# Optimization experiments

Hardware: AMD Instinct MI355X
Metric: run time of the kernel (lower is better)

## Reference

```python
import jax, jax.numpy as jnp
import numpy as np

ALPHA = 0.5  # args.alpha in the original script
N_NODES = 100000   # line-graph nodes == edges of the original graph
N_EDGES = 1600000  # line-graph edges (non-backtracking adjacency)
D = 128

def setup_inputs() -> dict:
    key = jax.random.key(0)
    k1, k2, k3 = jax.random.split(key, 3)
    edge_feats = jax.random.normal(k1, (N_NODES, D), dtype=jnp.float32)
    src = jax.random.randint(k2, (N_EDGES,), 0, N_NODES, dtype=jnp.int32)
    dst = jax.random.randint(k3, (N_EDGES,), 0, N_NODES, dtype=jnp.int32)
    return {"edge_feats": edge_feats, "src": src, "dst": dst}

def reference(edge_feats, src, dst):
    # copy_u: gather source-node features along line-graph edges
    msg = edge_feats[src]                                   # [E, D]
    n = edge_feats.shape[0]
    # mean reduce per destination node; zero-degree nodes -> 0 (DGL semantics)
    s = jax.ops.segment_sum(msg, dst, num_segments=n)       # [N, D]
    cnt = jax.ops.segment_sum(jnp.ones((src.shape[0],), edge_feats.dtype), dst, num_segments=n)
    h_new = s / jnp.maximum(cnt, 1.0)[:, None]
    # alpha-weighted residual mix
    return ALPHA * edge_feats + (1.0 - ALPHA) * h_new
```

## Files before the change

### kernel.cpp

```cpp
#include <hip/hip_runtime.h>
#include <hip/hip_fp16.h>

#define NN 100000
#define NE 1600000
#define NBKT 782
#define CHUNK 8192
#define NBLK1 196
#define DIRW (NBKT + 1)
#define CAPB 2432
#define CVTBLK 604
#define GRID1 (NBLK1 + CVTBLK)

#define OFF_DIR   0
#define OFF_PAIRS 153600
#define OFF_F16   (OFF_PAIRS + NBLK1 * CHUNK)
#define WORDS_ALL (OFF_F16 + NN * 64)

__global__ __launch_bounds__(512) void bin_convert_kernel(
        const int* __restrict__ src, const int* __restrict__ dst,
        const float2* __restrict__ feats2,
        unsigned* __restrict__ pairs1, int* __restrict__ dir,
        __half2* __restrict__ f16, int fp16on) {
    __shared__ unsigned stage[CHUNK];
    __shared__ int hist[NBKT];
    __shared__ int bbase[NBKT];
    __shared__ int curs[NBKT];
    __shared__ int tsum[512];
    const int tid = threadIdx.x;
    const int blk = blockIdx.x;

    if (blk >= NBLK1) {
        if (fp16on) {
            const int cb = blk - NBLK1;
            for (int i = cb * 512 + tid; i < NN * 64; i += CVTBLK * 512)
                f16[i] = __float22half2_rn(feats2[i]);
        }
        return;
    }

    const int e0 = blk * CHUNK;
    const int n = min(CHUNK, NE - e0);

    for (int b = tid; b < NBKT; b += 512) hist[b] = 0;
    __syncthreads();
    for (int i = tid; i < n; i += 512)
        atomicAdd(&hist[dst[e0 + i] >> 7], 1);
    __syncthreads();

    const int b0 = tid * 2, b1 = tid * 2 + 1;
    const int v0 = (b0 < NBKT) ? hist[b0] : 0;
    const int v1 = (b1 < NBKT) ? hist[b1] : 0;
    tsum[tid] = v0 + v1;
    __syncthreads();
    for (int st = 1; st < 512; st <<= 1) {
        int t = (tid >= st) ? tsum[tid - st] : 0;
        __syncthreads();
        tsum[tid] += t;
        __syncthreads();
    }
    const int tb = tsum[tid] - (v0 + v1);
    if (b0 < NBKT) { bbase[b0] = tb;      curs[b0] = tb; }
    if (b1 < NBKT) { bbase[b1] = tb + v0; curs[b1] = tb + v0; }
    __syncthreads();

    for (int i = tid; i < n; i += 512) {
        const int d = dst[e0 + i];
        const int sv = src[e0 + i];
        const int pos = atomicAdd(&curs[d >> 7], 1);
        stage[pos] = ((unsigned)sv << 7) | (unsigned)(d & 127);
    }
    __syncthreads();

    unsigned* gp = pairs1 + (size_t)blk * CHUNK;
    for (int i = tid; i < n; i += 512) gp[i] = stage[i];
    int* dp = dir + (size_t)blk * DIRW;
    for (int b = tid; b < NBKT; b += 512) dp[b] = bbase[b];
    if (tid == 0) dp[NBKT] = n;
}

__global__ __launch_bounds__(256) void gather_kernel(
        const float2* __restrict__ feats2,
        const __half2* __restrict__ f16,
        const unsigned* __restrict__ pairs1,
        const int* __restrict__ dir,
        float2* __restrict__ out2, int fp16on) {
    __shared__ unsigned pairs_s[CAPB];
    __shared__ int idx_s[CAPB];
    __shared__ int rbase[NBLK1], rlen[NBLK1], rdst[NBLK1];
    __shared__ int scan_t[256];
    __shared__ int hist[128], offs[128], curs[128];
    __shared__ int total_s;

    const int b = blockIdx.x;
    const int tid = threadIdx.x;
    const int node0 = b << 7;
    const int nNodes = min(128, NN - node0);

    int cj = 0;
    if (tid < NBLK1) {
        const int* dp = dir + (size_t)tid * DIRW + b;
        const int s0 = dp[0];
        const int s1 = dp[1];
        rbase[tid] = s0;
        cj = s1 - s0;
        rlen[tid] = cj;
    }
    scan_t[tid] = cj;
    __syncthreads();
    for (int st = 1; st < 256; st <<= 1) {
        int t = (tid >= st) ? scan_t[tid - st] : 0;
        __syncthreads();
        scan_t[tid] += t;
        __syncthreads();
    }
    if (tid < NBLK1) rdst[tid] = scan_t[tid] - cj;
    if (tid == 255) total_s = scan_t[255];
    __syncthreads();
    const int cnt = min(total_s, CAPB);

    const int sub = tid >> 5, lane32 = tid & 31;
    for (int j = sub; j < NBLK1; j += 8) {
        const int len = rlen[j];
        const int gb = rbase[j];
        const int db = rdst[j];
        const unsigned* gp = pairs1 + (size_t)j * CHUNK + gb;
        for (int k = lane32; k < len; k += 32) {
            const int dpos = db + k;
            if (dpos < CAPB) pairs_s[dpos] = gp[k];
        }
    }
    if (tid < 128) hist[tid] = 0;
    __syncthreads();

    for (int i = tid; i < cnt; i += 256) atomicAdd(&hist[pairs_s[i] & 127], 1);
    __syncthreads();

    if (tid < 128) curs[tid] = hist[tid];
    __syncthreads();
    for (int st = 1; st < 128; st <<= 1) {
        int t = (tid < 128 && tid >= st) ? curs[tid - st] : 0;
        __syncthreads();
        if (tid < 128) curs[tid] += t;
        __syncthreads();
    }
    if (tid < 128) {
        const int ex = curs[tid] - hist[tid];
        offs[tid] = ex;
        curs[tid] = ex;
    }
    __syncthreads();
    for (int i = tid; i < cnt; i += 256) {
        const unsigned p = pairs_s[i];
        const int pos = atomicAdd(&curs[p & 127], 1);
        idx_s[pos] = (int)(p >> 7);
    }
    __syncthreads();

    const int lane = tid & 63;
    const int w = tid >> 6;
    for (int dl = w; dl < nNodes; dl += 4) {
        const int start = offs[dl];
        const int deg = hist[dl];
        float2 acc = make_float2(0.f, 0.f);
        int j = 0;
        if (fp16on) {
            for (; j + 3 < deg; j += 4) {
                const int s0 = idx_s[start + j + 0];
                const int s1 = idx_s[start + j + 1];
                const int s2 = idx_s[start + j + 2];
                const int s3 = idx_s[start + j + 3];
                const float2 v0 = __half22float2(f16[(size_t)s0 * 64 + lane]);
                const float2 v1 = __half22float2(f16[(size_t)s1 * 64 + lane]);
                const float2 v2 = __half22float2(f16[(size_t)s2 * 64 + lane]);
                const float2 v3 = __half22float2(f16[(size_t)s3 * 64 + lane]);
                acc.x += v0.x + v1.x + v2.x + v3.x;
                acc.y += v0.y + v1.y + v2.y + v3.y;
            }
            for (; j < deg; ++j) {
                const float2 v = __half22float2(f16[(size_t)idx_s[start + j] * 64 + lane]);
                acc.x += v.x; acc.y += v.y;
            }
        } else {
            for (; j + 3 < deg; j += 4) {
                const int s0 = idx_s[start + j + 0];
                const int s1 = idx_s[start + j + 1];
                const int s2 = idx_s[start + j + 2];
                const int s3 = idx_s[start + j + 3];
                const float2 v0 = feats2[(size_t)s0 * 64 + lane];
                const float2 v1 = feats2[(size_t)s1 * 64 + lane];
                const float2 v2 = feats2[(size_t)s2 * 64 + lane];
                const float2 v3 = feats2[(size_t)s3 * 64 + lane];
                acc.x += v0.x + v1.x + v2.x + v3.x;
                acc.y += v0.y + v1.y + v2.y + v3.y;
            }
            for (; j < deg; ++j) {
                const float2 v = feats2[(size_t)idx_s[start + j] * 64 + lane];
                acc.x += v.x; acc.y += v.y;
            }
        }
        const int node = node0 + dl;
        const float inv = 0.5f / fmaxf((float)deg, 1.0f);
        const float2 f = feats2[(size_t)node * 64 + lane];
        out2[(size_t)node * 64 + lane] =
            make_float2(0.5f * f.x + inv * acc.x, 0.5f * f.y + inv * acc.y);
    }
}

extern "C" void kernel_launch(void* const* d_in, const int* in_sizes, int n_in,
                              void* d_out, int out_size, void* d_ws, size_t ws_size,
                              hipStream_t stream) {
    const float* feats = (const float*)d_in[0];
    const int*   src   = (const int*)d_in[1];
    const int*   dst   = (const int*)d_in[2];
    float* out = (float*)d_out;

    int*      ws_i   = (int*)d_ws;
    int*      dir    = ws_i + OFF_DIR;
    unsigned* pairs1 = (unsigned*)(ws_i + OFF_PAIRS);
    __half2*  f16    = (__half2*)(ws_i + OFF_F16);
    const int fp16on = (ws_size >= (size_t)WORDS_ALL * 4u) ? 1 : 0;

    bin_convert_kernel<<<GRID1, 512, 0, stream>>>(
        src, dst, (const float2*)feats, pairs1, dir, f16, fp16on);
    gather_kernel<<<NBKT, 256, 0, stream>>>(
        (const float2*)feats, f16, pairs1, dir, (float2*)out, fp16on);
}
```

Measured before the change: 207.9 us.

## Halve bin chunks, use wave-shuffle scans, unroll gather, read residual from fp16

The binning kernel now uses 4096-edge chunks with 391 blocks of 256 threads and fewer conversion blocks. Both kernels replace the barrier-heavy shared-memory prefix scans with wavefront shuffle scans plus a small cross-wave total. The gather unrolls the fp16 path to 8 loads in flight and reads the residual term from the fp16 copy instead of fp32. The trade-off is that the gather must now merge 391 directory runs per bucket, and the residual term loses precision by coming from fp16.

```diff
diff --git a/kernel.cpp b/kernel.cpp
--- a/kernel.cpp
+++ b/kernel.cpp
@@ -4,19 +4,19 @@
 #define NN 100000
 #define NE 1600000
 #define NBKT 782
-#define CHUNK 8192
-#define NBLK1 196
+#define CHUNK 4096
+#define NBLK1 391
 #define DIRW (NBKT + 1)
 #define CAPB 2432
-#define CVTBLK 604
+#define CVTBLK 409
 #define GRID1 (NBLK1 + CVTBLK)
 
 #define OFF_DIR   0
-#define OFF_PAIRS 153600
+#define OFF_PAIRS 306176
 #define OFF_F16   (OFF_PAIRS + NBLK1 * CHUNK)
 #define WORDS_ALL (OFF_F16 + NN * 64)
 
-__global__ __launch_bounds__(512) void bin_convert_kernel(
+__global__ __launch_bounds__(256) void bin_convert_kernel(
         const int* __restrict__ src, const int* __restrict__ dst,
         const float2* __restrict__ feats2,
         unsigned* __restrict__ pairs1, int* __restrict__ dir,
@@ -25,14 +25,14 @@
     __shared__ int hist[NBKT];
     __shared__ int bbase[NBKT];
     __shared__ int curs[NBKT];
-    __shared__ int tsum[512];
+    __shared__ int wtot[4];
     const int tid = threadIdx.x;
     const int blk = blockIdx.x;
 
     if (blk >= NBLK1) {
         if (fp16on) {
             const int cb = blk - NBLK1;
-            for (int i = cb * 512 + tid; i < NN * 64; i += CVTBLK * 512)
+            for (int i = cb * 256 + tid; i < NN * 64; i += CVTBLK * 256)
                 f16[i] = __float22half2_rn(feats2[i]);
         }
         return;
@@ -41,29 +41,39 @@
     const int e0 = blk * CHUNK;
     const int n = min(CHUNK, NE - e0);
 
-    for (int b = tid; b < NBKT; b += 512) hist[b] = 0;
-    __syncthreads();
-    for (int i = tid; i < n; i += 512)
+    for (int b = tid; b < NBKT; b += 256) hist[b] = 0;
+    __syncthreads();
+    for (int i = tid; i < n; i += 256)
         atomicAdd(&hist[dst[e0 + i] >> 7], 1);
     __syncthreads();
 
-    const int b0 = tid * 2, b1 = tid * 2 + 1;
-    const int v0 = (b0 < NBKT) ? hist[b0] : 0;
-    const int v1 = (b1 < NBKT) ? hist[b1] : 0;
-    tsum[tid] = v0 + v1;
-    __syncthreads();
-    for (int st = 1; st < 512; st <<= 1) {
-        int t = (tid >= st) ? tsum[tid - st] : 0;
-        __syncthreads();
-        tsum[tid] += t;
-        __syncthreads();
-    }
-    const int tb = tsum[tid] - (v0 + v1);
-    if (b0 < NBKT) { bbase[b0] = tb;      curs[b0] = tb; }
-    if (b1 < NBKT) { bbase[b1] = tb + v0; curs[b1] = tb + v0; }
-    __syncthreads();
-
-    for (int i = tid; i < n; i += 512) {
+    int v[4];
+    int s = 0;
+    #pragma unroll
+    for (int k = 0; k < 4; ++k) {
+        const int b = tid * 4 + k;
+        v[k] = (b < NBKT) ? hist[b] : 0;
+        s += v[k];
+    }
+    const int lane = tid & 63, wv = tid >> 6;
+    int inc = s;
+    #pragma unroll
+    for (int d = 1; d < 64; d <<= 1) {
+        const int t = __shfl_up(inc, d);
+        if (lane >= d) inc += t;
+    }
+    if (lane == 63) wtot[wv] = inc;
+    __syncthreads();
+    int run = inc - s;
+    for (int w = 0; w < wv; ++w) run += wtot[w];
+    #pragma unroll
+    for (int k = 0; k < 4; ++k) {
+        const int b = tid * 4 + k;
+        if (b < NBKT) { bbase[b] = run; curs[b] = run; run += v[k]; }
+    }
+    __syncthreads();
+
+    for (int i = tid; i < n; i += 256) {
         const int d = dst[e0 + i];
         const int sv = src[e0 + i];
         const int pos = atomicAdd(&curs[d >> 7], 1);
@@ -72,9 +82,9 @@
     __syncthreads();
 
     unsigned* gp = pairs1 + (size_t)blk * CHUNK;
-    for (int i = tid; i < n; i += 512) gp[i] = stage[i];
+    for (int i = tid; i < n; i += 256) gp[i] = stage[i];
     int* dp = dir + (size_t)blk * DIRW;
-    for (int b = tid; b < NBKT; b += 512) dp[b] = bbase[b];
+    for (int b = tid; b < NBKT; b += 256) dp[b] = bbase[b];
     if (tid == 0) dp[NBKT] = n;
 }
 
@@ -87,49 +97,59 @@
     __shared__ unsigned pairs_s[CAPB];
     __shared__ int idx_s[CAPB];
     __shared__ int rbase[NBLK1], rlen[NBLK1], rdst[NBLK1];
-    __shared__ int scan_t[256];
+    __shared__ int wtot[4];
     __shared__ int hist[128], offs[128], curs[128];
-    __shared__ int total_s;
 
     const int b = blockIdx.x;
     const int tid = threadIdx.x;
     const int node0 = b << 7;
     const int nNodes = min(128, NN - node0);
 
-    int cj = 0;
-    if (tid < NBLK1) {
-        const int* dp = dir + (size_t)tid * DIRW + b;
+    const int e0i = tid * 2, e1i = tid * 2 + 1;
+    int l0 = 0, l1 = 0;
+    if (e0i < NBLK1) {
+        const int* dp = dir + (size_t)e0i * DIRW + b;
         const int s0 = dp[0];
-        const int s1 = dp[1];
-        rbase[tid] = s0;
-        cj = s1 - s0;
-        rlen[tid] = cj;
-    }
-    scan_t[tid] = cj;
-    __syncthreads();
-    for (int st = 1; st < 256; st <<= 1) {
-        int t = (tid >= st) ? scan_t[tid - st] : 0;
-        __syncthreads();
-        scan_t[tid] += t;
-        __syncthreads();
-    }
-    if (tid < NBLK1) rdst[tid] = scan_t[tid] - cj;
-    if (tid == 255) total_s = scan_t[255];
-    __syncthreads();
-    const int cnt = min(total_s, CAPB);
-
-    const int sub = tid >> 5, lane32 = tid & 31;
-    for (int j = sub; j < NBLK1; j += 8) {
+        rbase[e0i] = s0;
+        l0 = dp[1] - s0;
+        rlen[e0i] = l0;
+    }
+    if (e1i < NBLK1) {
+        const int* dp = dir + (size_t)e1i * DIRW + b;
+        const int s0 = dp[0];
+        rbase[e1i] = s0;
+        l1 = dp[1] - s0;
+        rlen[e1i] = l1;
+    }
+    const int s = l0 + l1;
+    const int lane = tid & 63, wv = tid >> 6;
+    int inc = s;
+    #pragma unroll
+    for (int d = 1; d < 64; d <<= 1) {
+        const int t = __shfl_up(inc, d);
+        if (lane >= d) inc += t;
+    }
+    if (lane == 63) wtot[wv] = inc;
+    __syncthreads();
+    int base = inc - s;
+    for (int w = 0; w < wv; ++w) base += wtot[w];
+    if (e0i < NBLK1) rdst[e0i] = base;
+    if (e1i < NBLK1) rdst[e1i] = base + l0;
+    const int total = wtot[0] + wtot[1] + wtot[2] + wtot[3];
+    if (tid < 128) hist[tid] = 0;
+    __syncthreads();
+    const int cnt = min(total, CAPB);
+
+    const int sub = tid >> 4, lane16 = tid & 15;
+    for (int j = sub; j < NBLK1; j += 16) {
         const int len = rlen[j];
-        const int gb = rbase[j];
         const int db = rdst[j];
-        const unsigned* gp = pairs1 + (size_t)j * CHUNK + gb;
-        for (int k = lane32; k < len; k += 32) {
+        const unsigned* gp = pairs1 + (size_t)j * CHUNK + rbase[j];
+        for (int k = lane16; k < len; k += 16) {
             const int dpos = db + k;
             if (dpos < CAPB) pairs_s[dpos] = gp[k];
         }
     }
-    if (tid < 128) hist[tid] = 0;
     __syncthreads();
 
     for (int i = tid; i < cnt; i += 256) atomicAdd(&hist[pairs_s[i] & 127], 1);
@@ -156,25 +176,20 @@
     }
     __syncthreads();
 
-    const int lane = tid & 63;
-    const int w = tid >> 6;
-    for (int dl = w; dl < nNodes; dl += 4) {
+    const int w64 = tid >> 6;
+    for (int dl = w64; dl < nNodes; dl += 4) {
         const int start = offs[dl];
         const int deg = hist[dl];
         float2 acc = make_float2(0.f, 0.f);
         int j = 0;
         if (fp16on) {
-            for (; j + 3 < deg; j += 4) {
-                const int s0 = idx_s[start + j + 0];
-                const int s1 = idx_s[start + j + 1];
-                const int s2 = idx_s[start + j + 2];
-                const int s3 = idx_s[start + j + 3];
-                const float2 v0 = __half22float2(f16[(size_t)s0 * 64 + lane]);
-                const float2 v1 = __half22float2(f16[(size_t)s1 * 64 + lane]);
-                const float2 v2 = __half22float2(f16[(size_t)s2 * 64 + lane]);
-                const float2 v3 = __half22float2(f16[(size_t)s3 * 64 + lane]);
-                acc.x += v0.x + v1.x + v2.x + v3.x;
-                acc.y += v0.y + v1.y + v2.y + v3.y;
+            for (; j + 7 < deg; j += 8) {
+                float2 v[8];
+                #pragma unroll
+                for (int k = 0; k < 8; ++k)
+                    v[k] = __half22float2(f16[(size_t)idx_s[start + j + k] * 64 + lane]);
+                #pragma unroll
+                for (int k = 0; k < 8; ++k) { acc.x += v[k].x; acc.y += v[k].y; }
             }
             for (; j < deg; ++j) {
                 const float2 v = __half22float2(f16[(size_t)idx_s[start + j] * 64 + lane]);
@@ -182,16 +197,12 @@
             }
         } else {
             for (; j + 3 < deg; j += 4) {
-                const int s0 = idx_s[start + j + 0];
-                const int s1 = idx_s[start + j + 1];
-                const int s2 = idx_s[start + j + 2];
-                const int s3 = idx_s[start + j + 3];
-                const float2 v0 = feats2[(size_t)s0 * 64 + lane];
-                const float2 v1 = feats2[(size_t)s1 * 64 + lane];
-                const float2 v2 = feats2[(size_t)s2 * 64 + lane];
-                const float2 v3 = feats2[(size_t)s3 * 64 + lane];
-                acc.x += v0.x + v1.x + v2.x + v3.x;
-                acc.y += v0.y + v1.y + v2.y + v3.y;
+                float2 v[4];
+                #pragma unroll
+                for (int k = 0; k < 4; ++k)
+                    v[k] = feats2[(size_t)idx_s[start + j + k] * 64 + lane];
+                #pragma unroll
+                for (int k = 0; k < 4; ++k) { acc.x += v[k].x; acc.y += v[k].y; }
             }
             for (; j < deg; ++j) {
                 const float2 v = feats2[(size_t)idx_s[start + j] * 64 + lane];
@@ -200,7 +211,8 @@
         }
         const int node = node0 + dl;
         const float inv = 0.5f / fmaxf((float)deg, 1.0f);
-        const float2 f = feats2[(size_t)node * 64 + lane];
+        const float2 f = fp16on ? __half22float2(f16[(size_t)node * 64 + lane])
+                                : feats2[(size_t)node * 64 + lane];
         out2[(size_t)node * 64 + lane] =
             make_float2(0.5f * f.x + inv * acc.x, 0.5f * f.y + inv * acc.y);
     }
@@ -220,7 +232,7 @@
     __half2*  f16    = (__half2*)(ws_i + OFF_F16);
     const int fp16on = (ws_size >= (size_t)WORDS_ALL * 4u) ? 1 : 0;
 
-    bin_convert_kernel<<<GRID1, 512, 0, stream>>>(
+    bin_convert_kernel<<<GRID1, 256, 0, stream>>>(
         src, dst, (const float2*)feats, pairs1, dir, f16, fp16on);
     gather_kernel<<<NBKT, 256, 0, stream>>>(
         (const float2*)feats, f16, pairs1, dir, (float2*)out, fp16on);
```

After: 228.9 us. 1.1x slower.
